# Kernel tuning notes

Hardware: AMD Instinct MI355X
Metric: run time of the kernel (lower is better)

The kernel has to match this reference:

```python
import jax, jax.numpy as jnp
import numpy as np

HIDDEN = 1024
INTER = 4096
NUM_EXPERTS = 8
TOP_K = 2
BATCH, SEQ = 2, 1024


def setup_inputs() -> dict:
    key = jax.random.key(0)
    ks = jax.random.split(key, 5)
    s_h = 1.0 / np.sqrt(HIDDEN)
    s_f = 1.0 / np.sqrt(INTER)
    x = jax.random.normal(ks[0], (BATCH, SEQ, HIDDEN), dtype=jnp.float32)
    gate_w = jax.random.normal(ks[1], (HIDDEN, NUM_EXPERTS), dtype=jnp.float32) * s_h
    w_gate = jax.random.normal(ks[2], (NUM_EXPERTS, HIDDEN, INTER), dtype=jnp.float32) * s_h
    w_up = jax.random.normal(ks[3], (NUM_EXPERTS, HIDDEN, INTER), dtype=jnp.float32) * s_h
    w_down = jax.random.normal(ks[4], (NUM_EXPERTS, INTER, HIDDEN), dtype=jnp.float32) * s_f
    return {"x": x, "gate_w": gate_w, "w_gate": w_gate, "w_up": w_up, "w_down": w_down}


def reference(x, gate_w, w_gate, w_up, w_down):
    B, S, H = x.shape
    E = w_gate.shape[0]
    xf = x.reshape(-1, H)  # [T, H]

    # Router: softmax over experts, take top-k, then re-softmax the top-k PROBS
    # (the torch module applies softmax to the probabilities, not the logits).
    gate_probs = jax.nn.softmax(xf @ gate_w, axis=-1)          # [T, E]
    topk_p, topk_i = jax.lax.top_k(gate_probs, TOP_K)           # [T, K]
    topk_w = jax.nn.softmax(topk_p, axis=-1)                    # [T, K]

    # Combine weights per (token, expert): sum of topk weights routed to e.
    combine = jnp.einsum('tke,tk->te', jax.nn.one_hot(topk_i, E, dtype=xf.dtype), topk_w)  # [T, E]

    # Dense all-expert SwiGLU MLP, then weighted combine (same math as masked loop).
    g = jax.nn.silu(jnp.einsum('th,ehf->etf', xf, w_gate))      # [E, T, F]
    u = jnp.einsum('th,ehf->etf', xf, w_up)                     # [E, T, F]
    d = jnp.einsum('etf,efh->eth', g * u, w_down)               # [E, T, H]
    out = jnp.einsum('eth,te->th', d, combine)                  # [T, H]
    return out.reshape(B, S, H)
```

## Files before the change

### kernel.cpp

```cpp
#include <hip/hip_runtime.h>
#include <hip/hip_bf16.h>
#include <cstdint>


typedef short short8 __attribute__((ext_vector_type(8)));
typedef float floatx4 __attribute__((ext_vector_type(4)));

#define H_DIM 1024
#define F_DIM 4096
#define N_EXP 8
#define T_TOK 2048
#define MCAP  5120

#define BM 128
#define BN 64
#define BK 32
#define LDT 40

struct Meta {
  int cnt[N_EXP];
  int cursor[N_EXP];
  int poff[N_EXP + 1];
  int pad0;
  int pair_token[MCAP];
  float pair_w[MCAP];
  int token_pair[2 * T_TOK];
  int tok_e[2 * T_TOK];
  float tok_w[2 * T_TOK];
};

__device__ __forceinline__ unsigned short f2b(float f) {
  unsigned int u = __float_as_uint(f);
  u = (u + 0x7fffu + ((u >> 16) & 1u)) >> 16;
  return (unsigned short)u;
}
__device__ __forceinline__ float b2f(unsigned short h) {
  return __uint_as_float(((unsigned int)h) << 16);
}

__device__ __forceinline__ void gll16(const void* g, void* l) {
  __builtin_amdgcn_global_load_lds(
      (const __attribute__((address_space(1))) unsigned int*)g,
      (__attribute__((address_space(3))) unsigned int*)l, 16, 0, 0);
}

__global__ void k_init(Meta* __restrict__ m) {
  int i = threadIdx.x;
  if (i < N_EXP) { m->cnt[i] = 0; m->cursor[i] = 0; }
}

__global__ __launch_bounds__(64)
void k_router(const float* __restrict__ x, const float* __restrict__ gw,
              Meta* __restrict__ m) {
  int t = blockIdx.x;
  int lane = threadIdx.x;
  const float* xr = x + (size_t)t * H_DIM;
  float acc[N_EXP];
#pragma unroll
  for (int e = 0; e < N_EXP; ++e) acc[e] = 0.f;
  for (int i = 0; i < H_DIM / 64; ++i) {
    int h = i * 64 + lane;
    float xv = xr[h];
    const float* g = gw + (size_t)h * N_EXP;
#pragma unroll
    for (int e = 0; e < N_EXP; ++e) acc[e] += xv * g[e];
  }
#pragma unroll
  for (int e = 0; e < N_EXP; ++e) {
    float v = acc[e];
    for (int off = 32; off; off >>= 1) v += __shfl_xor(v, off, 64);
    acc[e] = v;
  }
  if (lane == 0) {
    float mx = acc[0];
    for (int e = 1; e < N_EXP; ++e) mx = fmaxf(mx, acc[e]);
    float p[N_EXP];
    float s = 0.f;
    for (int e = 0; e < N_EXP; ++e) { p[e] = __expf(acc[e] - mx); s += p[e]; }
    float inv = 1.f / s;
    for (int e = 0; e < N_EXP; ++e) p[e] *= inv;
    int i1 = 0;
    for (int e = 1; e < N_EXP; ++e) if (p[e] > p[i1]) i1 = e;
    int i2 = (i1 == 0) ? 1 : 0;
    for (int e = 0; e < N_EXP; ++e) if (e != i1 && p[e] > p[i2]) i2 = e;
    float w1 = 1.f / (1.f + __expf(p[i2] - p[i1]));
    m->tok_e[2 * t] = i1;     m->tok_e[2 * t + 1] = i2;
    m->tok_w[2 * t] = w1;     m->tok_w[2 * t + 1] = 1.f - w1;
    atomicAdd(&m->cnt[i1], 1);
    atomicAdd(&m->cnt[i2], 1);
  }
}

__global__ void k_scan(Meta* __restrict__ m) {
  if (threadIdx.x == 0 && blockIdx.x == 0) {
    int o = 0;
    for (int e = 0; e < N_EXP; ++e) {
      m->poff[e] = o;
      o += ((m->cnt[e] + BM - 1) / BM) * BM;
    }
    m->poff[N_EXP] = o;
  }
}

__global__ void k_assign(Meta* __restrict__ m) {
  int t = blockIdx.x * blockDim.x + threadIdx.x;
  if (t >= T_TOK) return;
  for (int k = 0; k < 2; ++k) {
    int e = m->tok_e[2 * t + k];
    int idx = atomicAdd(&m->cursor[e], 1);
    int p = m->poff[e] + idx;
    m->pair_token[p] = t;
    m->pair_w[p] = m->tok_w[2 * t + k];
    m->token_pair[2 * t + k] = p;
  }
}

__global__ __launch_bounds__(256)
void k_gather(const float* __restrict__ x, unsigned short* __restrict__ Xe,
              const Meta* __restrict__ m) {
  int r = blockIdx.x;
  if (r >= m->poff[N_EXP]) return;
  int e = 0;
#pragma unroll
  for (int i = 1; i < N_EXP; ++i) if (r >= m->poff[i]) e = i;
  bool real = (r - m->poff[e]) < m->cnt[e];
  int h = threadIdx.x * 4;
  ushort4 sv = {0, 0, 0, 0};
  if (real) {
    int t = m->pair_token[r];
    float4 f = *(const float4*)(x + (size_t)t * H_DIM + h);
    sv.x = f2b(f.x); sv.y = f2b(f.y); sv.z = f2b(f.z); sv.w = f2b(f.w);
  }
  *(ushort4*)(Xe + (size_t)r * H_DIM + h) = sv;
}

__global__ __launch_bounds__(256)
void k_prep(const float* __restrict__ W, unsigned short* __restrict__ Wt,
            int K, int NT, int N) {
  __shared__ __align__(16) unsigned short Ls[2048];
  int e = blockIdx.y, nt = blockIdx.x;
  int t = threadIdx.x;
  int KB = K >> 5;
  int kb0 = blockIdx.z * 32;
  int kb1 = kb0 + 32;
  int k = t >> 3;
  int nc = (t & 7) * 8;
  for (int kb = kb0; kb < kb1; ++kb) {
    const float* src = W + ((size_t)e * K + (size_t)kb * 32 + k) * N + (size_t)nt * 64 + nc;
    float4 f0 = *(const float4*)src;
    float4 f1 = *(const float4*)(src + 4);
    Ls[(nc + 0) * 32 + k] = f2b(f0.x);
    Ls[(nc + 1) * 32 + k] = f2b(f0.y);
    Ls[(nc + 2) * 32 + k] = f2b(f0.z);
    Ls[(nc + 3) * 32 + k] = f2b(f0.w);
    Ls[(nc + 4) * 32 + k] = f2b(f1.x);
    Ls[(nc + 5) * 32 + k] = f2b(f1.y);
    Ls[(nc + 6) * 32 + k] = f2b(f1.z);
    Ls[(nc + 7) * 32 + k] = f2b(f1.w);
    __syncthreads();
    short8 v = *(const short8*)&Ls[t * 8];
    size_t dst = (((size_t)e * NT + nt) * KB + kb) * 2048 + (size_t)t * 8;
    *(short8*)&Wt[dst] = v;
    __syncthreads();
  }
}

__global__ __launch_bounds__(256, 2)
void k_gemm_dual2(const unsigned short* __restrict__ Xe,
                  const unsigned short* __restrict__ WtG,
                  const unsigned short* __restrict__ WtU,
                  unsigned short* __restrict__ Aw,
                  const Meta* __restrict__ m) {
  __shared__ __align__(16) unsigned short As[BM * 32];
  __shared__ __align__(16) unsigned short Bg[BN * 32];
  __shared__ __align__(16) unsigned short Bu[BN * 32];
  int tileM = blockIdx.y * BM;
  if (tileM >= m->poff[N_EXP]) return;
  int e = 0;
#pragma unroll
  for (int i = 1; i < N_EXP; ++i) if (tileM >= m->poff[i]) e = i;
  int nt = blockIdx.x;
  int n0 = nt * BN;

  int tid = threadIdx.x;
  int lane = tid & 63;
  int wid = tid >> 6;
  int wm = (wid & 1) * 64;
  int wn = (wid >> 1) * 32;
  int lm = lane & 15;
  int quad = lane >> 4;

  floatx4 accG[4][2] = {};
  floatx4 accU[4][2] = {};

  int c0 = wid * 128 + lane;
  int c1 = c0 + 64;
  int bc = wid * 64 + lane;

  for (int k0 = 0; k0 < H_DIM; k0 += BK) {
    int kb = k0 >> 5;
    size_t btile = (((size_t)e * (F_DIM / 64) + nt) * (H_DIM / 32) + kb) * 2048;
    gll16(Xe + (size_t)(tileM + (c0 >> 2)) * H_DIM + k0 + (c0 & 3) * 8, &As[wid * 1024]);
    gll16(Xe + (size_t)(tileM + (c1 >> 2)) * H_DIM + k0 + (c1 & 3) * 8, &As[wid * 1024 + 512]);
    gll16(WtG + btile + (size_t)bc * 8, &Bg[wid * 512]);
    gll16(WtU + btile + (size_t)bc * 8, &Bu[wid * 512]);
    __syncthreads();
    short8 a[4];
#pragma unroll
    for (int fm = 0; fm < 4; ++fm)
      a[fm] = *(const short8*)&As[(wm + fm * 16 + lm) * 32 + quad * 8];
#pragma unroll
    for (int fn = 0; fn < 2; ++fn) {
      short8 bg = *(const short8*)&Bg[(wn + fn * 16 + lm) * 32 + quad * 8];
      short8 bu = *(const short8*)&Bu[(wn + fn * 16 + lm) * 32 + quad * 8];
#pragma unroll
      for (int fm = 0; fm < 4; ++fm) {
        accG[fm][fn] = __builtin_amdgcn_mfma_f32_16x16x32_bf16(a[fm], bg, accG[fm][fn], 0, 0, 0);
        accU[fm][fn] = __builtin_amdgcn_mfma_f32_16x16x32_bf16(a[fm], bu, accU[fm][fn], 0, 0, 0);
      }
    }
    __syncthreads();
  }
#pragma unroll
  for (int fm = 0; fm < 4; ++fm)
#pragma unroll
    for (int fn = 0; fn < 2; ++fn)
#pragma unroll
      for (int r = 0; r < 4; ++r) {
        int row = tileM + wm + fm * 16 + quad * 4 + r;
        int col = n0 + wn + fn * 16 + lm;
        float g = accG[fm][fn][r];
        float u = accU[fm][fn][r];
        float s = g / (1.f + __expf(-g));
        Aw[(size_t)row * F_DIM + col] = f2b(s * u);
      }
}

__global__ __launch_bounds__(256, 2)
void k_gemm_down2(const unsigned short* __restrict__ Aw,
                  const unsigned short* __restrict__ WtD,
                  unsigned short* __restrict__ Y,
                  const Meta* __restrict__ m) {
  __shared__ __align__(16) unsigned short As[BM * 32];
  __shared__ __align__(16) unsigned short Bs[BN * 32];
  int tileM = blockIdx.y * BM;
  if (tileM >= m->poff[N_EXP]) return;
  int e = 0;
#pragma unroll
  for (int i = 1; i < N_EXP; ++i) if (tileM >= m->poff[i]) e = i;
  int nt = blockIdx.x;
  int n0 = nt * BN;

  int tid = threadIdx.x;
  int lane = tid & 63;
  int wid = tid >> 6;
  int wm = (wid & 1) * 64;
  int wn = (wid >> 1) * 32;
  int lm = lane & 15;
  int quad = lane >> 4;

  floatx4 acc[4][2] = {};

  int c0 = wid * 128 + lane;
  int c1 = c0 + 64;
  int bc = wid * 64 + lane;

  for (int k0 = 0; k0 < F_DIM; k0 += BK) {
    int kb = k0 >> 5;
    size_t btile = (((size_t)e * (H_DIM / 64) + nt) * (F_DIM / 32) + kb) * 2048;
    gll16(Aw + (size_t)(tileM + (c0 >> 2)) * F_DIM + k0 + (c0 & 3) * 8, &As[wid * 1024]);
    gll16(Aw + (size_t)(tileM + (c1 >> 2)) * F_DIM + k0 + (c1 & 3) * 8, &As[wid * 1024 + 512]);
    gll16(WtD + btile + (size_t)bc * 8, &Bs[wid * 512]);
    __syncthreads();
    short8 a[4];
#pragma unroll
    for (int fm = 0; fm < 4; ++fm)
      a[fm] = *(const short8*)&As[(wm + fm * 16 + lm) * 32 + quad * 8];
#pragma unroll
    for (int fn = 0; fn < 2; ++fn) {
      short8 b = *(const short8*)&Bs[(wn + fn * 16 + lm) * 32 + quad * 8];
#pragma unroll
      for (int fm = 0; fm < 4; ++fm)
        acc[fm][fn] = __builtin_amdgcn_mfma_f32_16x16x32_bf16(a[fm], b, acc[fm][fn], 0, 0, 0);
    }
    __syncthreads();
  }
#pragma unroll
  for (int fm = 0; fm < 4; ++fm)
#pragma unroll
    for (int fn = 0; fn < 2; ++fn)
#pragma unroll
      for (int r = 0; r < 4; ++r) {
        int row = tileM + wm + fm * 16 + quad * 4 + r;
        int col = n0 + wn + fn * 16 + lm;
        Y[(size_t)row * H_DIM + col] = f2b(acc[fm][fn][r]);
      }
}

__global__ __launch_bounds__(256, 2)
void k_gemm_dual_fb(const unsigned short* __restrict__ Xe,
                    const float* __restrict__ w_gate,
                    const float* __restrict__ w_up,
                    unsigned short* __restrict__ Aw,
                    const Meta* __restrict__ m) {
  __shared__ unsigned short As[BM * LDT];
  __shared__ unsigned short Bg[BN * LDT];
  __shared__ unsigned short Bu[BN * LDT];
  int tileM = blockIdx.y * BM;
  if (tileM >= m->poff[N_EXP]) return;
  int e = 0;
#pragma unroll
  for (int i = 1; i < N_EXP; ++i) if (tileM >= m->poff[i]) e = i;
  int n0 = blockIdx.x * BN;
  const float* Wg = w_gate + (size_t)e * H_DIM * F_DIM;
  const float* Wu = w_up   + (size_t)e * H_DIM * F_DIM;
  int tid = threadIdx.x;
  int lane = tid & 63;
  int wid = tid >> 6;
  int wm = (wid & 1) * 64;
  int wn = (wid >> 1) * 32;
  int lm = lane & 15;
  int quad = lane >> 4;
  floatx4 accG[4][2] = {};
  floatx4 accU[4][2] = {};
  for (int k0 = 0; k0 < H_DIM; k0 += BK) {
    {
      int c = tid;
#pragma unroll
      for (int it = 0; it < 2; ++it, c += 256) {
        int row = c >> 2, kp = c & 3;
        *(uint4*)&As[row * LDT + kp * 8] =
            *(const uint4*)(Xe + (size_t)(tileM + row) * H_DIM + k0 + kp * 8);
      }
    }
    {
      int nn = tid & 63;
      int kh = tid >> 6;
      const float* sg = Wg + (size_t)(k0 + kh * 8) * F_DIM + n0 + nn;
      const float* su = Wu + (size_t)(k0 + kh * 8) * F_DIM + n0 + nn;
      short8 vg, vu;
#pragma unroll
      for (int j = 0; j < 8; ++j) {
        vg[j] = (short)f2b(sg[(size_t)j * F_DIM]);
        vu[j] = (short)f2b(su[(size_t)j * F_DIM]);
      }
      *(short8*)&Bg[nn * LDT + kh * 8] = vg;
      *(short8*)&Bu[nn * LDT + kh * 8] = vu;
    }
    __syncthreads();
    short8 a[4];
#pragma unroll
    for (int fm = 0; fm < 4; ++fm)
      a[fm] = *(const short8*)&As[(wm + fm * 16 + lm) * LDT + quad * 8];
#pragma unroll
    for (int fn = 0; fn < 2; ++fn) {
      short8 bg = *(const short8*)&Bg[(wn + fn * 16 + lm) * LDT + quad * 8];
      short8 bu = *(const short8*)&Bu[(wn + fn * 16 + lm) * LDT + quad * 8];
#pragma unroll
      for (int fm = 0; fm < 4; ++fm) {
        accG[fm][fn] = __builtin_amdgcn_mfma_f32_16x16x32_bf16(a[fm], bg, accG[fm][fn], 0, 0, 0);
        accU[fm][fn] = __builtin_amdgcn_mfma_f32_16x16x32_bf16(a[fm], bu, accU[fm][fn], 0, 0, 0);
      }
    }
    __syncthreads();
  }
#pragma unroll
  for (int fm = 0; fm < 4; ++fm)
#pragma unroll
    for (int fn = 0; fn < 2; ++fn)
#pragma unroll
      for (int r = 0; r < 4; ++r) {
        int row = tileM + wm + fm * 16 + quad * 4 + r;
        int col = n0 + wn + fn * 16 + lm;
        float g = accG[fm][fn][r];
        float u = accU[fm][fn][r];
        float s = g / (1.f + __expf(-g));
        Aw[(size_t)row * F_DIM + col] = f2b(s * u);
      }
}

__global__ __launch_bounds__(256, 2)
void k_gemm_down_fb(const unsigned short* __restrict__ Aw,
                    const float* __restrict__ w_down,
                    unsigned short* __restrict__ Y,
                    const Meta* __restrict__ m) {
  __shared__ unsigned short As[BM * LDT];
  __shared__ unsigned short Bs[BN * LDT];
  int tileM = blockIdx.y * BM;
  if (tileM >= m->poff[N_EXP]) return;
  int e = 0;
#pragma unroll
  for (int i = 1; i < N_EXP; ++i) if (tileM >= m->poff[i]) e = i;
  int n0 = blockIdx.x * BN;
  const float* W = w_down + (size_t)e * F_DIM * H_DIM;
  int tid = threadIdx.x;
  int lane = tid & 63;
  int wid = tid >> 6;
  int wm = (wid & 1) * 64;
  int wn = (wid >> 1) * 32;
  int lm = lane & 15;
  int quad = lane >> 4;
  floatx4 acc[4][2] = {};
  for (int k0 = 0; k0 < F_DIM; k0 += BK) {
    {
      int c = tid;
#pragma unroll
      for (int it = 0; it < 2; ++it, c += 256) {
        int row = c >> 2, kp = c & 3;
        *(uint4*)&As[row * LDT + kp * 8] =
            *(const uint4*)(Aw + (size_t)(tileM + row) * F_DIM + k0 + kp * 8);
      }
    }
    {
      int nn = tid & 63;
      int kh = tid >> 6;
      const float* s = W + (size_t)(k0 + kh * 8) * H_DIM + n0 + nn;
      short8 v;
#pragma unroll
      for (int j = 0; j < 8; ++j) v[j] = (short)f2b(s[(size_t)j * H_DIM]);
      *(short8*)&Bs[nn * LDT + kh * 8] = v;
    }
    __syncthreads();
    short8 a[4];
#pragma unroll
    for (int fm = 0; fm < 4; ++fm)
      a[fm] = *(const short8*)&As[(wm + fm * 16 + lm) * LDT + quad * 8];
#pragma unroll
    for (int fn = 0; fn < 2; ++fn) {
      short8 b = *(const short8*)&Bs[(wn + fn * 16 + lm) * LDT + quad * 8];
#pragma unroll
      for (int fm = 0; fm < 4; ++fm)
        acc[fm][fn] = __builtin_amdgcn_mfma_f32_16x16x32_bf16(a[fm], b, acc[fm][fn], 0, 0, 0);
    }
    __syncthreads();
  }
#pragma unroll
  for (int fm = 0; fm < 4; ++fm)
#pragma unroll
    for (int fn = 0; fn < 2; ++fn)
#pragma unroll
      for (int r = 0; r < 4; ++r) {
        int row = tileM + wm + fm * 16 + quad * 4 + r;
        int col = n0 + wn + fn * 16 + lm;
        Y[(size_t)row * H_DIM + col] = f2b(acc[fm][fn][r]);
      }
}

__global__ __launch_bounds__(256)
void k_combine(const unsigned short* __restrict__ Y, const Meta* __restrict__ m,
               float* __restrict__ out) {
  int t = blockIdx.x;
  int h = threadIdx.x * 4;
  int p0 = m->token_pair[2 * t];
  int p1 = m->token_pair[2 * t + 1];
  float w0 = m->pair_w[p0];
  float w1 = m->pair_w[p1];
  ushort4 y0 = *(const ushort4*)(Y + (size_t)p0 * H_DIM + h);
  ushort4 y1 = *(const ushort4*)(Y + (size_t)p1 * H_DIM + h);
  float4 o;
  o.x = w0 * b2f(y0.x) + w1 * b2f(y1.x);
  o.y = w0 * b2f(y0.y) + w1 * b2f(y1.y);
  o.z = w0 * b2f(y0.z) + w1 * b2f(y1.z);
  o.w = w0 * b2f(y0.w) + w1 * b2f(y1.w);
  *(float4*)(out + (size_t)t * H_DIM + h) = o;
}

extern "C" void kernel_launch(void* const* d_in, const int* in_sizes, int n_in,
                              void* d_out, int out_size, void* d_ws, size_t ws_size,
                              hipStream_t stream) {
  const float* x  = (const float*)d_in[0];
  const float* gw = (const float*)d_in[1];
  const float* wg = (const float*)d_in[2];
  const float* wu = (const float*)d_in[3];
  const float* wd = (const float*)d_in[4];
  float* out = (float*)d_out;

  unsigned short* Xe = (unsigned short*)d_ws;
  unsigned short* Aw = Xe + (size_t)MCAP * H_DIM;
  unsigned short* Y  = Aw + (size_t)MCAP * F_DIM;
  Meta* m = (Meta*)(Y + (size_t)MCAP * H_DIM);
  uintptr_t wtp = ((uintptr_t)(m + 1) + 255) & ~(uintptr_t)255;
  unsigned short* WtG = (unsigned short*)wtp;
  const size_t WSZ = (size_t)N_EXP * H_DIM * F_DIM;
  unsigned short* WtU = WtG + WSZ;
  unsigned short* WtD = WtU + WSZ;
  size_t need = (size_t)((char*)(WtD + WSZ) - (char*)d_ws);
  bool big = ws_size >= need;

  k_init<<<1, 64, 0, stream>>>(m);
  k_router<<<T_TOK, 64, 0, stream>>>(x, gw, m);
  k_scan<<<1, 64, 0, stream>>>(m);
  k_assign<<<T_TOK / 256, 256, 0, stream>>>(m);
  k_gather<<<MCAP, 256, 0, stream>>>(x, Xe, m);

  if (big) {
    k_prep<<<dim3(F_DIM / 64, N_EXP, 1), 256, 0, stream>>>(wg, WtG, H_DIM, F_DIM / 64, F_DIM);
    k_prep<<<dim3(F_DIM / 64, N_EXP, 1), 256, 0, stream>>>(wu, WtU, H_DIM, F_DIM / 64, F_DIM);
    k_prep<<<dim3(H_DIM / 64, N_EXP, 4), 256, 0, stream>>>(wd, WtD, F_DIM, H_DIM / 64, H_DIM);
    k_gemm_dual2<<<dim3(F_DIM / BN, MCAP / BM), 256, 0, stream>>>(Xe, WtG, WtU, Aw, m);
    k_gemm_down2<<<dim3(H_DIM / BN, MCAP / BM), 256, 0, stream>>>(Aw, WtD, Y, m);
  } else {
    k_gemm_dual_fb<<<dim3(F_DIM / BN, MCAP / BM), 256, 0, stream>>>(Xe, wg, wu, Aw, m);
    k_gemm_down_fb<<<dim3(H_DIM / BN, MCAP / BM), 256, 0, stream>>>(Aw, wd, Y, m);
  }
  k_combine<<<T_TOK, 256, 0, stream>>>(Y, m, out);
}
```

Before: 699.0 us.

## Rewrite weight prep without LDS, split K across more blocks, raise occupancy

Replaces the LDS-transposing weight conversion kernel with one where each thread reads eight strided floats directly and writes a packed bf16 vector, removing shared memory and barriers. The K dimension is split across many more blocks (4 k-blocks each) to expose more parallelism for the conversion pass, which dominates memory traffic. The GEMM kernels' launch bounds are raised to 4 waves per SIMD, which may force register spilling. The strided global reads are less coalesced per thread but still cover contiguous columns across lanes.

```diff
diff --git a/kernel.cpp b/kernel.cpp
--- a/kernel.cpp
+++ b/kernel.cpp
@@ -134,38 +134,32 @@
   *(ushort4*)(Xe + (size_t)r * H_DIM + h) = sv;
 }
 
-__global__ __launch_bounds__(256)
-void k_prep(const float* __restrict__ W, unsigned short* __restrict__ Wt,
-            int K, int NT, int N) {
-  __shared__ __align__(16) unsigned short Ls[2048];
+__global__ __launch_bounds__(256, 4)
+void k_prep2(const float* __restrict__ W, unsigned short* __restrict__ Wt,
+             int K, int NT, int N, int KB_PER) {
   int e = blockIdx.y, nt = blockIdx.x;
   int t = threadIdx.x;
+  int wid = t >> 6, lane = t & 63;
+  int dn = lane >> 2, k8 = lane & 3;
+  int n = wid * 16 + dn;
   int KB = K >> 5;
-  int kb0 = blockIdx.z * 32;
-  int kb1 = kb0 + 32;
-  int k = t >> 3;
-  int nc = (t & 7) * 8;
-  for (int kb = kb0; kb < kb1; ++kb) {
-    const float* src = W + ((size_t)e * K + (size_t)kb * 32 + k) * N + (size_t)nt * 64 + nc;
-    float4 f0 = *(const float4*)src;
-    float4 f1 = *(const float4*)(src + 4);
-    Ls[(nc + 0) * 32 + k] = f2b(f0.x);
-    Ls[(nc + 1) * 32 + k] = f2b(f0.y);
-    Ls[(nc + 2) * 32 + k] = f2b(f0.z);
-    Ls[(nc + 3) * 32 + k] = f2b(f0.w);
-    Ls[(nc + 4) * 32 + k] = f2b(f1.x);
-    Ls[(nc + 5) * 32 + k] = f2b(f1.y);
-    Ls[(nc + 6) * 32 + k] = f2b(f1.z);
-    Ls[(nc + 7) * 32 + k] = f2b(f1.w);
-    __syncthreads();
-    short8 v = *(const short8*)&Ls[t * 8];
+  int kb0 = blockIdx.z * KB_PER;
+  for (int i = 0; i < KB_PER; ++i) {
+    int kb = kb0 + i;
+    const float* src = W + ((size_t)e * K + (size_t)kb * 32 + k8 * 8) * N
+                         + (size_t)nt * 64 + n;
+    float v[8];
+#pragma unroll
+    for (int j = 0; j < 8; ++j) v[j] = src[(size_t)j * N];
+    short8 o;
+#pragma unroll
+    for (int j = 0; j < 8; ++j) o[j] = (short)f2b(v[j]);
     size_t dst = (((size_t)e * NT + nt) * KB + kb) * 2048 + (size_t)t * 8;
-    *(short8*)&Wt[dst] = v;
-    __syncthreads();
-  }
-}
-
-__global__ __launch_bounds__(256, 2)
+    *(short8*)&Wt[dst] = o;
+  }
+}
+
+__global__ __launch_bounds__(256, 4)
 void k_gemm_dual2(const unsigned short* __restrict__ Xe,
                   const unsigned short* __restrict__ WtG,
                   const unsigned short* __restrict__ WtU,
@@ -236,7 +230,7 @@
       }
 }
 
-__global__ __launch_bounds__(256, 2)
+__global__ __launch_bounds__(256, 4)
 void k_gemm_down2(const unsigned short* __restrict__ Aw,
                   const unsigned short* __restrict__ WtD,
                   unsigned short* __restrict__ Y,
@@ -494,9 +488,9 @@
   k_gather<<<MCAP, 256, 0, stream>>>(x, Xe, m);
 
   if (big) {
-    k_prep<<<dim3(F_DIM / 64, N_EXP, 1), 256, 0, stream>>>(wg, WtG, H_DIM, F_DIM / 64, F_DIM);
-    k_prep<<<dim3(F_DIM / 64, N_EXP, 1), 256, 0, stream>>>(wu, WtU, H_DIM, F_DIM / 64, F_DIM);
-    k_prep<<<dim3(H_DIM / 64, N_EXP, 4), 256, 0, stream>>>(wd, WtD, F_DIM, H_DIM / 64, H_DIM);
+    k_prep2<<<dim3(F_DIM / 64, N_EXP, 8), 256, 0, stream>>>(wg, WtG, H_DIM, F_DIM / 64, F_DIM, 4);
+    k_prep2<<<dim3(F_DIM / 64, N_EXP, 8), 256, 0, stream>>>(wu, WtU, H_DIM, F_DIM / 64, F_DIM, 4);
+    k_prep2<<<dim3(H_DIM / 64, N_EXP, 32), 256, 0, stream>>>(wd, WtD, F_DIM, H_DIM / 64, H_DIM, 4);
     k_gemm_dual2<<<dim3(F_DIM / BN, MCAP / BM), 256, 0, stream>>>(Xe, WtG, WtU, Aw, m);
     k_gemm_down2<<<dim3(H_DIM / BN, MCAP / BM), 256, 0, stream>>>(Aw, WtD, Y, m);
   } else {
```

Result: no change. 697.5 us (-0.2%).
